# Performance work log

Hardware: AMD Instinct MI355X
Metric: run time of the kernel (lower is better)

## Reference

```python
import jax, jax.numpy as jnp
import numpy as np

N = 10000   # num_nodes
P = 32      # input_dim
Q = 64      # output_dim
K = 2       # diffusion_steps
B = 32      # batch
E = 160000  # edges per transition matrix (avg degree 16)
M = 2 * K + 1  # num_matrices (dual random walk)


def setup_inputs() -> dict:
    key = jax.random.key(0)
    ks = jax.random.split(key, 8)
    inputs = jax.random.normal(ks[0], (B, N * P), dtype=jnp.float32)
    trans1_idx = jax.random.randint(ks[1], (2, E), 0, N, dtype=jnp.int32)
    trans1_val = jax.random.uniform(ks[2], (E,), dtype=jnp.float32)
    trans2_idx = jax.random.randint(ks[3], (2, E), 0, N, dtype=jnp.int32)
    trans2_val = jax.random.uniform(ks[4], (E,), dtype=jnp.float32)
    weight = jax.random.normal(ks[5], (P * M, Q), dtype=jnp.float32) * (1.414 / np.sqrt(P * M))
    bias = jnp.zeros((Q,), dtype=jnp.float32)
    return {"inputs": inputs, "trans1_idx": trans1_idx, "trans1_val": trans1_val,
            "trans2_idx": trans2_idx, "trans2_val": trans2_val,
            "weight": weight, "bias": bias}


def _spmm(idx, val, x):
    # sparse [N,N] (COO rows=idx[0], cols=idx[1]) @ dense x [N, F]
    gathered = val[:, None] * x[idx[1]]            # [E, F]
    return jax.ops.segment_sum(gathered, idx[0], num_segments=N)


def reference(inputs, trans1_idx, trans1_val, trans2_idx, trans2_val, weight, bias):
    batch_size = inputs.shape[0]
    # [B, N*P] -> [N, P*B] (matches torch transpose/reshape sequence)
    x0_base = inputs.reshape(batch_size, N, P).transpose(1, 2, 0).reshape(N, P * batch_size)
    xs = [x0_base]
    for idx, val in ((trans1_idx, trans1_val), (trans2_idx, trans2_val)):
        x0 = x0_base
        x1 = _spmm(idx, val, x0)
        xs.append(x1)
        for _ in range(2, K + 1):
            x2 = 2.0 * _spmm(idx, val, x1) - x0
            xs.append(x2)
            x1, x0 = x2, x1
    x = jnp.stack(xs)                                   # [M, N, P*B]
    x = x.reshape(M, N, P, batch_size).transpose(3, 1, 2, 0)  # [B, N, P, M]
    x = x.reshape(batch_size * N, P * M)
    out = x @ weight + bias                             # [B*N, Q]
    return out.reshape(batch_size, N * Q)
```

## Files before the change

### kernel.cpp

```cpp
#include <hip/hip_runtime.h>
#include <hip/hip_bf16.h>

#define NN 10000
#define PP 32
#define QQ 64
#define EE 160000
#define FF 1024
#define NQ 640000
#define SLOTS 64

typedef __attribute__((ext_vector_type(8))) short sh8;
typedef __attribute__((ext_vector_type(8))) __bf16 bf8v;
typedef __attribute__((ext_vector_type(4))) float f32x4;

__device__ __forceinline__ short f2bf(float f) {
    return __builtin_bit_cast(short, __float2bfloat16(f));
}

__global__ __launch_bounds__(256)
void pre_kernel(const float* __restrict__ in, short* __restrict__ x0,
                const float* __restrict__ W, short* __restrict__ wt,
                int* __restrict__ cnt, int2* __restrict__ ed1, int2* __restrict__ ed2) {
    int t = threadIdx.x;
    if (blockIdx.x == 0) {
#pragma unroll
        for (int j = 0; j < 40; ++j) {
            int idx = t + j * 256;
            int k = idx >> 6, q = idx & 63;
            int p = k / 5;
            int m = k - p * 5;
            wt[q * 160 + m * 32 + p] = f2bf(W[idx]);
        }
        return;
    }
    int n = blockIdx.x - 1;
    int b = t >> 3;
    int p0 = (t & 7) * 4;
    float4 v = *(const float4*)(in + (size_t)b * (NN * PP) + (size_t)n * PP + p0);
    short4 s = make_short4(f2bf(v.x), f2bf(v.y), f2bf(v.z), f2bf(v.w));
    *(short4*)(x0 + (size_t)n * FF + b * 32 + p0) = s;
    if (t < 32)      *(int4*)(ed1 + n * SLOTS + t * 2) = make_int4(0, 0, 0, 0);
    else if (t < 64) *(int4*)(ed2 + n * SLOTS + (t - 32) * 2) = make_int4(0, 0, 0, 0);
    else if (t == 64) { cnt[n] = 0; cnt[NN + n] = 0; }
}

__global__ __launch_bounds__(256)
void scatter_kernel(const int* __restrict__ t1i, const float* __restrict__ t1v,
                    const int* __restrict__ t2i, const float* __restrict__ t2v,
                    int* __restrict__ cnt, int2* __restrict__ ed1, int2* __restrict__ ed2) {
    int tid = blockIdx.x * 256 + threadIdx.x;
    const int* idx; const float* val; int* cn; int2* ed; int e0;
    if (tid < EE / 2) { idx = t1i; val = t1v; cn = cnt;      ed = ed1; e0 = tid * 2; }
    else              { idx = t2i; val = t2v; cn = cnt + NN; ed = ed2; e0 = (tid - EE / 2) * 2; }
    int2 rr = *(const int2*)(idx + e0);
    int2 cc = *(const int2*)(idx + EE + e0);
    float2 vv = *(const float2*)(val + e0);
    int pos0 = atomicAdd(&cn[rr.x], 1);
    if (pos0 < SLOTS) ed[rr.x * SLOTS + pos0] = make_int2(cc.x, __float_as_int(vv.x));
    int pos1 = atomicAdd(&cn[rr.y], 1);
    if (pos1 < SLOTS) ed[rr.y * SLOTS + pos1] = make_int2(cc.y, __float_as_int(vv.y));
}

__global__ __launch_bounds__(256)
void spmm_kernel(const int* __restrict__ cnt, const int2* __restrict__ ed1,
                 const int2* __restrict__ ed2,
                 const short* __restrict__ x1s, const short* __restrict__ x2s,
                 short* __restrict__ out1, short* __restrict__ out2,
                 const short* __restrict__ sub, float alpha) {
    int bid = blockIdx.x;
    int c = bid & 7;
    int rest = bid >> 3;
    int rb = rest % 625;
    int g = rest / 625;
    int fbase = c * 128;
    int wid  = threadIdx.x >> 6;
    int lane = threadIdx.x & 63;
    int grp  = lane >> 4;
    int l8   = (lane & 15) * 8;
    int n = rb * 16 + wid * 4 + grp;

    const char* edb; const char* xb; short* out; int cn;
    if (g == 0) { edb = (const char*)ed1; xb = (const char*)x1s; out = out1; cn = cnt[n]; }
    else        { edb = (const char*)ed2; xb = (const char*)x2s; out = out2; cn = cnt[NN + n]; }
    xb += (unsigned)fbase * 2;
    cn = min(cn, SLOTS);
    int iters = (cn + 7) >> 3;
    unsigned eoff = (unsigned)n * (SLOTS * 8);
    unsigned voff = (unsigned)l8 * 2;

    float acc[8];
#pragma unroll
    for (int j = 0; j < 8; ++j) acc[j] = 0.f;

    int4 e0 = *(const int4*)(edb + eoff);
    int4 e1 = *(const int4*)(edb + eoff + 16);
    int4 e2 = *(const int4*)(edb + eoff + 32);
    int4 e3 = *(const int4*)(edb + eoff + 48);

    for (int it = 0; it < iters; ++it) {
        bf8v g0 = *(const bf8v*)(xb + (((unsigned)e0.x << 11) | voff));
        bf8v g1 = *(const bf8v*)(xb + (((unsigned)e0.z << 11) | voff));
        bf8v g2 = *(const bf8v*)(xb + (((unsigned)e1.x << 11) | voff));
        bf8v g3 = *(const bf8v*)(xb + (((unsigned)e1.z << 11) | voff));
        bf8v g4 = *(const bf8v*)(xb + (((unsigned)e2.x << 11) | voff));
        bf8v g5 = *(const bf8v*)(xb + (((unsigned)e2.z << 11) | voff));
        bf8v g6 = *(const bf8v*)(xb + (((unsigned)e3.x << 11) | voff));
        bf8v g7 = *(const bf8v*)(xb + (((unsigned)e3.z << 11) | voff));
        eoff += 64;
        int4 f0 = *(const int4*)(edb + eoff);
        int4 f1 = *(const int4*)(edb + eoff + 16);
        int4 f2 = *(const int4*)(edb + eoff + 32);
        int4 f3 = *(const int4*)(edb + eoff + 48);
        float v0 = __int_as_float(e0.y), v1 = __int_as_float(e0.w);
        float v2 = __int_as_float(e1.y), v3 = __int_as_float(e1.w);
        float v4 = __int_as_float(e2.y), v5 = __int_as_float(e2.w);
        float v6 = __int_as_float(e3.y), v7 = __int_as_float(e3.w);
#pragma unroll
        for (int j = 0; j < 8; ++j) {
            acc[j] = fmaf((float)g0[j], v0, acc[j]);
            acc[j] = fmaf((float)g1[j], v1, acc[j]);
            acc[j] = fmaf((float)g2[j], v2, acc[j]);
            acc[j] = fmaf((float)g3[j], v3, acc[j]);
            acc[j] = fmaf((float)g4[j], v4, acc[j]);
            acc[j] = fmaf((float)g5[j], v5, acc[j]);
            acc[j] = fmaf((float)g6[j], v6, acc[j]);
            acc[j] = fmaf((float)g7[j], v7, acc[j]);
        }
        e0 = f0; e1 = f1; e2 = f2; e3 = f3;
    }

    size_t obase = (size_t)n * FF + fbase + l8;
    sh8 o;
    if (sub) {
        bf8v s = *(const bf8v*)((const __bf16*)sub + obase);
#pragma unroll
        for (int j = 0; j < 8; ++j) o[j] = f2bf(alpha * acc[j] - (float)s[j]);
    } else {
#pragma unroll
        for (int j = 0; j < 8; ++j) o[j] = f2bf(acc[j]);
    }
    *(sh8*)(out + obase) = o;
}

__global__ __launch_bounds__(256)
void gemm_mfma_kernel(const short* __restrict__ xs, const short* __restrict__ wt,
                      const float* __restrict__ bias, float* __restrict__ out) {
    int t = threadIdx.x;
    int lane = t & 63;
    int gw = blockIdx.x * 4 + (t >> 6);
    int c = lane & 15, hi = lane >> 4;

    sh8 a0[5], a1[5], a2[5], a3[5];
#pragma unroll
    for (int ks = 0; ks < 5; ++ks) {
        a0[ks] = *(const sh8*)(wt + (0 * 16 + c) * 160 + ks * 32 + hi * 8);
        a1[ks] = *(const sh8*)(wt + (1 * 16 + c) * 160 + ks * 32 + hi * 8);
        a2[ks] = *(const sh8*)(wt + (2 * 16 + c) * 160 + ks * 32 + hi * 8);
        a3[ks] = *(const sh8*)(wt + (3 * 16 + c) * 160 + ks * 32 + hi * 8);
    }
    float4 bv0 = *(const float4*)(bias + 0 * 16 + hi * 4);
    float4 bv1 = *(const float4*)(bias + 1 * 16 + hi * 4);
    float4 bv2 = *(const float4*)(bias + 2 * 16 + hi * 4);
    float4 bv3 = *(const float4*)(bias + 3 * 16 + hi * 4);

    for (int item = gw; item < 20000; item += 5000) {
        int b = item & 31, nt = item >> 5;
        const short* base = xs + (size_t)(nt * 16 + c) * FF + b * 32 + hi * 8;
        f32x4 acc0 = {0.f, 0.f, 0.f, 0.f};
        f32x4 acc1 = {0.f, 0.f, 0.f, 0.f};
        f32x4 acc2 = {0.f, 0.f, 0.f, 0.f};
        f32x4 acc3 = {0.f, 0.f, 0.f, 0.f};
#pragma unroll
        for (int ks = 0; ks < 5; ++ks) {
            sh8 bf = *(const sh8*)(base + (size_t)ks * ((size_t)NN * FF));
            acc0 = __builtin_amdgcn_mfma_f32_16x16x32_bf16(a0[ks], bf, acc0, 0, 0, 0);
            acc1 = __builtin_amdgcn_mfma_f32_16x16x32_bf16(a1[ks], bf, acc1, 0, 0, 0);
            acc2 = __builtin_amdgcn_mfma_f32_16x16x32_bf16(a2[ks], bf, acc2, 0, 0, 0);
            acc3 = __builtin_amdgcn_mfma_f32_16x16x32_bf16(a3[ks], bf, acc3, 0, 0, 0);
        }
        float* po = out + (size_t)b * NQ + (size_t)(nt * 16 + c) * 64 + hi * 4;
        *(float4*)(po +  0) = make_float4(acc0[0] + bv0.x, acc0[1] + bv0.y, acc0[2] + bv0.z, acc0[3] + bv0.w);
        *(float4*)(po + 16) = make_float4(acc1[0] + bv1.x, acc1[1] + bv1.y, acc1[2] + bv1.z, acc1[3] + bv1.w);
        *(float4*)(po + 32) = make_float4(acc2[0] + bv2.x, acc2[1] + bv2.y, acc2[2] + bv2.z, acc2[3] + bv2.w);
        *(float4*)(po + 48) = make_float4(acc3[0] + bv3.x, acc3[1] + bv3.y, acc3[2] + bv3.z, acc3[3] + bv3.w);
    }
}

extern "C" void kernel_launch(void* const* d_in, const int* in_sizes, int n_in,
                              void* d_out, int out_size, void* d_ws, size_t ws_size,
                              hipStream_t stream) {
    const float* inputs = (const float*)d_in[0];
    const int*   t1i    = (const int*)d_in[1];
    const float* t1v    = (const float*)d_in[2];
    const int*   t2i    = (const int*)d_in[3];
    const float* t2v    = (const float*)d_in[4];
    const float* W      = (const float*)d_in[5];
    const float* bias   = (const float*)d_in[6];
    float* out = (float*)d_out;

    short* ws = (short*)d_ws;
    const size_t NF = (size_t)NN * FF;
    short* x0  = ws;
    short* xs1 = ws + 1 * NF;
    short* xs2 = ws + 2 * NF;
    short* xs3 = ws + 3 * NF;
    short* xs4 = ws + 4 * NF;
    short* wt  = ws + 5 * NF;
    int* cnt  = (int*)(wt + 64 * 160);
    int2* ed1 = (int2*)(cnt + 2 * NN);
    int2* ed2 = ed1 + (size_t)NN * SLOTS;

    pre_kernel<<<NN + 1, 256, 0, stream>>>(inputs, x0, W, wt, cnt, ed1, ed2);
    scatter_kernel<<<EE / 256, 256, 0, stream>>>(t1i, t1v, t2i, t2v, cnt, ed1, ed2);

    const int spmm_grid = 2 * 625 * 8;

    spmm_kernel<<<spmm_grid, 256, 0, stream>>>(cnt, ed1, ed2,
                                               x0, x0, xs1, xs3,
                                               nullptr, 1.0f);
    spmm_kernel<<<spmm_grid, 256, 0, stream>>>(cnt, ed1, ed2,
                                               xs1, xs3, xs2, xs4,
                                               x0, 2.0f);

    gemm_mfma_kernel<<<1250, 256, 0, stream>>>(ws, wt, bias, out);
}
```

Before: 171.8 us.

## Assign one wave per SpMM row and split its edges across lane groups

The SpMM kernel now gives each wavefront a single output row instead of four. The four 16-lane groups of that wave take interleaved edges, one gathered bf16 vector per iteration, and are combined at the end with cross-lane xor shuffles. Because the loop count now depends on one row's degree and is made wave-uniform, waves no longer stall on the highest-degree row among four. The cost is a 4x larger grid, fewer independent gathers in flight per lane, extra shuffle reductions, and only one group doing the final store.

```diff
diff --git a/kernel.cpp b/kernel.cpp
--- a/kernel.cpp
+++ b/kernel.cpp
@@ -70,76 +70,59 @@
     int bid = blockIdx.x;
     int c = bid & 7;
     int rest = bid >> 3;
-    int rb = rest % 625;
-    int g = rest / 625;
+    int rb = rest % 2500;
+    int g = rest / 2500;
     int fbase = c * 128;
     int wid  = threadIdx.x >> 6;
     int lane = threadIdx.x & 63;
     int grp  = lane >> 4;
-    int l8   = (lane & 15) * 8;
-    int n = rb * 16 + wid * 4 + grp;
+    unsigned l16 = (unsigned)(lane & 15) * 16;
+    int n = rb * 4 + wid;
 
     const char* edb; const char* xb; short* out; int cn;
     if (g == 0) { edb = (const char*)ed1; xb = (const char*)x1s; out = out1; cn = cnt[n]; }
     else        { edb = (const char*)ed2; xb = (const char*)x2s; out = out2; cn = cnt[NN + n]; }
     xb += (unsigned)fbase * 2;
-    cn = min(cn, SLOTS);
-    int iters = (cn + 7) >> 3;
-    unsigned eoff = (unsigned)n * (SLOTS * 8);
-    unsigned voff = (unsigned)l8 * 2;
+    cn = __builtin_amdgcn_readfirstlane(min(cn, SLOTS));
+    int iters = (cn + 3) >> 2;
+
+    unsigned eoff = (unsigned)n * (SLOTS * 8) + (unsigned)grp * 8;
 
     float acc[8];
 #pragma unroll
     for (int j = 0; j < 8; ++j) acc[j] = 0.f;
 
-    int4 e0 = *(const int4*)(edb + eoff);
-    int4 e1 = *(const int4*)(edb + eoff + 16);
-    int4 e2 = *(const int4*)(edb + eoff + 32);
-    int4 e3 = *(const int4*)(edb + eoff + 48);
-
+    int2 cur = *(const int2*)(edb + eoff);
     for (int it = 0; it < iters; ++it) {
-        bf8v g0 = *(const bf8v*)(xb + (((unsigned)e0.x << 11) | voff));
-        bf8v g1 = *(const bf8v*)(xb + (((unsigned)e0.z << 11) | voff));
-        bf8v g2 = *(const bf8v*)(xb + (((unsigned)e1.x << 11) | voff));
-        bf8v g3 = *(const bf8v*)(xb + (((unsigned)e1.z << 11) | voff));
-        bf8v g4 = *(const bf8v*)(xb + (((unsigned)e2.x << 11) | voff));
-        bf8v g5 = *(const bf8v*)(xb + (((unsigned)e2.z << 11) | voff));
-        bf8v g6 = *(const bf8v*)(xb + (((unsigned)e3.x << 11) | voff));
-        bf8v g7 = *(const bf8v*)(xb + (((unsigned)e3.z << 11) | voff));
-        eoff += 64;
-        int4 f0 = *(const int4*)(edb + eoff);
-        int4 f1 = *(const int4*)(edb + eoff + 16);
-        int4 f2 = *(const int4*)(edb + eoff + 32);
-        int4 f3 = *(const int4*)(edb + eoff + 48);
-        float v0 = __int_as_float(e0.y), v1 = __int_as_float(e0.w);
-        float v2 = __int_as_float(e1.y), v3 = __int_as_float(e1.w);
-        float v4 = __int_as_float(e2.y), v5 = __int_as_float(e2.w);
-        float v6 = __int_as_float(e3.y), v7 = __int_as_float(e3.w);
-#pragma unroll
-        for (int j = 0; j < 8; ++j) {
-            acc[j] = fmaf((float)g0[j], v0, acc[j]);
-            acc[j] = fmaf((float)g1[j], v1, acc[j]);
-            acc[j] = fmaf((float)g2[j], v2, acc[j]);
-            acc[j] = fmaf((float)g3[j], v3, acc[j]);
-            acc[j] = fmaf((float)g4[j], v4, acc[j]);
-            acc[j] = fmaf((float)g5[j], v5, acc[j]);
-            acc[j] = fmaf((float)g6[j], v6, acc[j]);
-            acc[j] = fmaf((float)g7[j], v7, acc[j]);
+        int2 nxt = *(const int2*)(edb + eoff + 32);
+        eoff += 32;
+        bf8v xv = *(const bf8v*)(xb + ((((unsigned)cur.x) << 11) | l16));
+        float v = __int_as_float(cur.y);
+#pragma unroll
+        for (int j = 0; j < 8; ++j)
+            acc[j] = fmaf((float)xv[j], v, acc[j]);
+        cur = nxt;
+    }
+
+#pragma unroll
+    for (int j = 0; j < 8; ++j) {
+        acc[j] += __shfl_xor(acc[j], 16, 64);
+        acc[j] += __shfl_xor(acc[j], 32, 64);
+    }
+
+    if (grp == 0) {
+        size_t obase = (size_t)n * FF + fbase + (l16 >> 1);
+        sh8 o;
+        if (sub) {
+            bf8v s = *(const bf8v*)((const __bf16*)sub + obase);
+#pragma unroll
+            for (int j = 0; j < 8; ++j) o[j] = f2bf(alpha * acc[j] - (float)s[j]);
+        } else {
+#pragma unroll
+            for (int j = 0; j < 8; ++j) o[j] = f2bf(acc[j]);
         }
-        e0 = f0; e1 = f1; e2 = f2; e3 = f3;
-    }
-
-    size_t obase = (size_t)n * FF + fbase + l8;
-    sh8 o;
-    if (sub) {
-        bf8v s = *(const bf8v*)((const __bf16*)sub + obase);
-#pragma unroll
-        for (int j = 0; j < 8; ++j) o[j] = f2bf(alpha * acc[j] - (float)s[j]);
-    } else {
-#pragma unroll
-        for (int j = 0; j < 8; ++j) o[j] = f2bf(acc[j]);
-    }
-    *(sh8*)(out + obase) = o;
+        *(sh8*)(out + obase) = o;
+    }
 }
 
 __global__ __launch_bounds__(256)
@@ -213,7 +196,7 @@
     pre_kernel<<<NN + 1, 256, 0, stream>>>(inputs, x0, W, wt, cnt, ed1, ed2);
     scatter_kernel<<<EE / 256, 256, 0, stream>>>(t1i, t1v, t2i, t2v, cnt, ed1, ed2);
 
-    const int spmm_grid = 2 * 625 * 8;
+    const int spmm_grid = 2 * 2500 * 8;
 
     spmm_kernel<<<spmm_grid, 256, 0, stream>>>(cnt, ed1, ed2,
                                                x0, x0, xs1, xs3,
```

Result: slower. 230.6 us (+34.2%).
